# Kernel optimization log

Hardware: AMD Instinct MI355X
Metric: run time of the kernel (lower is better)

Reference implementation:

```python
import jax, jax.numpy as jnp
import numpy as np

N = 20        # number_of_nodes
K = 2         # Chebyshev order
E_DIM = 4     # embedding_dimensions
OUT = 2       # out_channels
F_IN = 8      # node_features
B = 131072    # batch


def setup_inputs() -> dict:
    key = jax.random.key(0)
    ks = jax.random.split(key, 8)
    x = jax.random.normal(ks[0], (B, N, F_IN), jnp.float32)
    e = jax.random.normal(ks[1], (N, E_DIM), jnp.float32)
    # AVWGCN parameter pools: weights_pool (E_DIM, K, in, out), bias_pool (E_DIM, out)
    gate_w = jax.random.normal(ks[2], (E_DIM, K, F_IN + OUT, 2 * OUT), jnp.float32) * 0.1
    gate_b = jax.random.normal(ks[3], (E_DIM, 2 * OUT), jnp.float32) * 0.1
    upd_w = jax.random.normal(ks[4], (E_DIM, K, F_IN + OUT, OUT), jnp.float32) * 0.1
    upd_b = jax.random.normal(ks[5], (E_DIM, OUT), jnp.float32) * 0.1
    lin_w = jax.random.normal(ks[6], (1, OUT), jnp.float32) * 0.5
    lin_b = jax.random.normal(ks[7], (1,), jnp.float32) * 0.1
    return {"x": x, "e": e, "gate_w": gate_w, "gate_b": gate_b,
            "upd_w": upd_w, "upd_b": upd_b, "lin_w": lin_w, "lin_b": lin_b}


def _avwgcn(x, e, supports, w_pool, b_pool):
    # Node-adaptive weights: (N, K, in, out) and bias (N, out)
    W = jnp.einsum('nd,dkio->nkio', e, w_pool)
    b = e @ b_pool
    # K-hop graph conv gather: (B, N, K, in)
    x_g = jnp.einsum('knm,bmc->bnkc', supports, x)
    return jnp.einsum('bnki,nkio->bno', x_g, W) + b


def reference(x, e, gate_w, gate_b, upd_w, upd_b, lin_w, lin_b):
    dt = x.dtype
    # Adaptive adjacency: softmax(relu(E E^T)) rows; Chebyshev set for K=2 is [I, A]
    A = jax.nn.softmax(jax.nn.relu(e @ e.T), axis=1)
    supports = jnp.stack([jnp.eye(N, dtype=dt), A.astype(dt)])  # (K, N, N)

    H = jnp.zeros((x.shape[0], N, OUT), dt)  # self.h is None -> zeros
    XH = jnp.concatenate([x, H], axis=-1)
    ZR = jax.nn.sigmoid(_avwgcn(XH, e, supports, gate_w, gate_b))
    Z, R = ZR[..., :OUT], ZR[..., OUT:]
    C = jnp.concatenate([x, Z * H], axis=-1)
    HC = jnp.tanh(_avwgcn(C, e, supports, upd_w, upd_b))
    H = R * H + (1.0 - R) * HC

    y = jax.nn.relu(H)
    y = y @ lin_w.T + lin_b
    return y
```

## Files before the change

### kernel.cpp

```cpp
#include <hip/hip_runtime.h>
#include <math.h>

#define NN 20
#define ED 4
#define XROW 160
#define NC 80
#define NKT 5
#define NNT 5
#define FRAG_BYTES (NKT * NNT * 64 * 16)
#define THREADS 512
#define ROWS_PER_WAVE 16
#define ROWS_PER_BLOCK 128
#define TPB 2

typedef __attribute__((ext_vector_type(8))) _Float16 half8;
typedef __attribute__((ext_vector_type(4))) float f32x4;
typedef __attribute__((ext_vector_type(4))) unsigned uint4v;

static __device__ __forceinline__ half8 cvt8(float4 a, float4 b) {
    uint4v u = (uint4v){
        __builtin_bit_cast(unsigned, __builtin_amdgcn_cvt_pkrtz(a.x, a.y)),
        __builtin_bit_cast(unsigned, __builtin_amdgcn_cvt_pkrtz(a.z, a.w)),
        __builtin_bit_cast(unsigned, __builtin_amdgcn_cvt_pkrtz(b.x, b.y)),
        __builtin_bit_cast(unsigned, __builtin_amdgcn_cvt_pkrtz(b.z, b.w))};
    return __builtin_bit_cast(half8, u);
}

static __device__ __forceinline__ float dpp_xor1(float v) {
    return __builtin_bit_cast(float,
        __builtin_amdgcn_mov_dpp(__builtin_bit_cast(int, v), 0xB1, 0xF, 0xF, true));
}
static __device__ __forceinline__ float dpp_xor2(float v) {
    return __builtin_bit_cast(float,
        __builtin_amdgcn_mov_dpp(__builtin_bit_cast(int, v), 0x4E, 0xF, 0xF, true));
}

struct Burst {
    float4 a0, b0, a1, b1, a2, b2, a3, b3, a4, b4;
};

static __device__ __forceinline__ Burst load_burst(const float* __restrict__ p) {
    Burst r;
    r.a0 = *(const float4*)(p);        r.b0 = *(const float4*)(p + 16);
    r.a1 = *(const float4*)(p + 32);   r.b1 = *(const float4*)(p + 48);
    r.a2 = *(const float4*)(p + 64);   r.b2 = *(const float4*)(p + 80);
    r.a3 = *(const float4*)(p + 96);   r.b3 = *(const float4*)(p + 112);
    r.a4 = *(const float4*)(p + 128);  r.b4 = *(const float4*)(p + 144);
    return r;
}

__global__ __launch_bounds__(THREADS, 4) void rgcn_fused(
        const float* __restrict__ x,
        const float* __restrict__ e,
        const float* __restrict__ gate_w,
        const float* __restrict__ gate_b,
        const float* __restrict__ upd_w,
        const float* __restrict__ upd_b,
        const float* __restrict__ lin_w,
        const float* __restrict__ lin_b,
        float* __restrict__ y) {
    __shared__ __align__(16) char fragmem[FRAG_BYTES];
    __shared__ float sbias[NC];
    __shared__ float el[80];
    __shared__ float sA[400];
    __shared__ float wself[640];
    __shared__ float wagg[640];

    const int t = threadIdx.x;
    const int l = t & 63;
    const int w = t >> 6;

    const size_t rowA = ((size_t)blockIdx.x * TPB + 0) * ROWS_PER_BLOCK + (size_t)w * ROWS_PER_WAVE;
    const size_t rowB = ((size_t)blockIdx.x * TPB + 1) * ROWS_PER_BLOCK + (size_t)w * ROWS_PER_WAVE;
    const float* xpA = x + (rowA + (l & 15)) * XROW + ((l >> 4) << 2);
    const float* xpB = x + (rowB + (l & 15)) * XROW + ((l >> 4) << 2);

    Burst bA = load_burst(xpA);

    if (t < NN * ED) el[t] = e[t];
    __syncthreads();

    if (t < 400) {
        int nn = t / 20, mm = t - (t / 20) * 20;
        float d = 0.f;
        #pragma unroll
        for (int j = 0; j < ED; ++j) d += el[nn * ED + j] * el[mm * ED + j];
        sA[t] = fmaxf(d, 0.f);
    }
    #pragma unroll
    for (int idx = t; idx < 1280; idx += THREADS) {
        int sel = idx >= 640;
        int rem = sel ? idx - 640 : idx;
        int c = rem >> 3, i = rem & 7;
        int n = c >> 2, ro = c & 3;
        float v = 0.f;
        if (ro < 2) {
            int o = 2 + ro;
            #pragma unroll
            for (int d = 0; d < ED; ++d) v += el[n * ED + d] * gate_w[d * 80 + sel * 40 + i * 4 + o];
        } else {
            int o = ro - 2;
            #pragma unroll
            for (int d = 0; d < ED; ++d) v += el[n * ED + d] * upd_w[d * 40 + sel * 20 + i * 2 + o];
        }
        (sel ? wagg : wself)[rem] = v;
    }
    if (t < NC) {
        int n = t >> 2, ro = t & 3;
        float b = 0.f;
        #pragma unroll
        for (int d = 0; d < ED; ++d)
            b += el[n * ED + d] * (ro < 2 ? gate_b[d * 4 + 2 + ro] : upd_b[d * 2 + ro - 2]);
        sbias[t] = b;
    }
    __syncthreads();

    if (t < NN) {
        float mx = -1e30f;
        for (int m = 0; m < NN; ++m) mx = fmaxf(mx, sA[t * 20 + m]);
        float ex[NN]; float sum = 0.f;
        for (int m = 0; m < NN; ++m) { ex[m] = __expf(sA[t * 20 + m] - mx); sum += ex[m]; }
        float inv = 1.f / sum;
        for (int m = 0; m < NN; ++m) sA[t * 20 + m] = ex[m] * inv;
    }
    __syncthreads();

    {
        half8* frag = (half8*)fragmem;
        const int gg = l >> 4;
        for (int tile = w; tile < NKT * NNT; tile += 8) {
            int kt = tile / 5, nt = tile - kt * 5;
            int cc = nt * 16 + (l & 15);
            int nn = cc >> 2;
            half8 hv;
            #pragma unroll
            for (int j = 0; j < 8; ++j) {
                int kk = (j < 4) ? (gg * 4 + j) : (16 + gg * 4 + (j - 4));
                int k = kt * 32 + kk;
                int m = k >> 3, i = k & 7;
                float val = sA[nn * 20 + m] * wagg[cc * 8 + i]
                          + (nn == m ? wself[cc * 8 + i] : 0.f);
                hv[j] = (_Float16)val;
            }
            frag[tile * 64 + l] = hv;
        }
    }
    __syncthreads();

    const half8* frag = (const half8*)fragmem;
    const float lw0 = lin_w[0], lw1 = lin_w[1], lb = lin_b[0];
    const int ro = l & 3;
    const bool isR = ro < 2;
    const float myw = (ro & 1) ? lw1 : lw0;

    Burst bB = load_burst(xpB);

    #define STEP(XA, XB, KT, ACC)                                                   \
    {                                                                               \
        half8 a = cvt8(XA, XB);                                                     \
        _Pragma("unroll")                                                           \
        for (int nt = 0; nt < NNT; ++nt) {                                          \
            half8 bh = frag[((KT) * NNT + nt) * 64 + l];                            \
            ACC[nt] = __builtin_amdgcn_mfma_f32_16x16x32_f16(a, bh, ACC[nt], 0, 0, 0); \
        }                                                                           \
    }

    #define EPILOGUE(ACC, ROW0)                                                     \
    {                                                                               \
        const size_t rowb = (ROW0) + ((l >> 4) << 2) + ro;                          \
        _Pragma("unroll")                                                           \
        for (int nt = 0; nt < NNT; ++nt) {                                          \
            const int n = nt * 4 + ((l & 15) >> 2);                                 \
            float ysel = 0.f;                                                       \
            _Pragma("unroll")                                                       \
            for (int q = 0; q < 4; ++q) {                                           \
                float pre = ACC[nt][q];                                             \
                float term;                                                         \
                if (isR) term = __builtin_amdgcn_rcpf(1.f + __expf(pre));           \
                else     term = 1.f - 2.f * __builtin_amdgcn_rcpf(__expf(2.f * pre) + 1.f); \
                float other = dpp_xor2(term);                                       \
                float h = term * other;                                             \
                float s = fmaxf(h, 0.f) * myw;                                      \
                float yq = s + dpp_xor1(s) + lb;                                    \
                if (q == ro) ysel = yq;                                             \
            }                                                                       \
            y[rowb * NN + n] = ysel;                                                \
        }                                                                           \
    }

    {
        f32x4 accA[NNT];
        #pragma unroll
        for (int nt = 0; nt < NNT; ++nt) {
            float b = sbias[nt * 16 + (l & 15)];
            accA[nt] = (f32x4){b, b, b, b};
        }
        STEP(bA.a0, bA.b0, 0, accA)
        STEP(bA.a1, bA.b1, 1, accA)
        STEP(bA.a2, bA.b2, 2, accA)
        STEP(bA.a3, bA.b3, 3, accA)
        STEP(bA.a4, bA.b4, 4, accA)
        EPILOGUE(accA, rowA)
    }

    {
        f32x4 accB[NNT];
        #pragma unroll
        for (int nt = 0; nt < NNT; ++nt) {
            float b = sbias[nt * 16 + (l & 15)];
            accB[nt] = (f32x4){b, b, b, b};
        }
        STEP(bB.a0, bB.b0, 0, accB)
        STEP(bB.a1, bB.b1, 1, accB)
        STEP(bB.a2, bB.b2, 2, accB)
        STEP(bB.a3, bB.b3, 3, accB)
        STEP(bB.a4, bB.b4, 4, accB)
        EPILOGUE(accB, rowB)
    }
    #undef STEP
    #undef EPILOGUE
}

extern "C" void kernel_launch(void* const* d_in, const int* in_sizes, int n_in,
                              void* d_out, int out_size, void* d_ws, size_t ws_size,
                              hipStream_t stream) {
    const float* x      = (const float*)d_in[0];
    const float* e      = (const float*)d_in[1];
    const float* gate_w = (const float*)d_in[2];
    const float* gate_b = (const float*)d_in[3];
    const float* upd_w  = (const float*)d_in[4];
    const float* upd_b  = (const float*)d_in[5];
    const float* lin_w  = (const float*)d_in[6];
    const float* lin_b  = (const float*)d_in[7];
    float* y = (float*)d_out;

    const int Bn = in_sizes[0] / XROW;
    const int nblocks = Bn / (ROWS_PER_BLOCK * TPB);

    rgcn_fused<<<nblocks, THREADS, 0, stream>>>(x, e, gate_w, gate_b,
                                                upd_w, upd_b, lin_w, lin_b, y);
}
```

Measured before the change: 25.43 us.

## Overlap x loads and weight prefetch with setup using no-drain barriers

```diff
diff --git a/kernel.cpp b/kernel.cpp
--- a/kernel.cpp
+++ b/kernel.cpp
@@ -35,17 +35,24 @@
         __builtin_amdgcn_mov_dpp(__builtin_bit_cast(int, v), 0x4E, 0xF, 0xF, true));
 }
 
+#define BARRIER_NODRAIN()                                   \
+    do {                                                    \
+        asm volatile("s_waitcnt lgkmcnt(0)" ::: "memory");  \
+        __builtin_amdgcn_s_barrier();                       \
+        __builtin_amdgcn_sched_barrier(0);                  \
+    } while (0)
+
 struct Burst {
     float4 a0, b0, a1, b1, a2, b2, a3, b3, a4, b4;
 };
 
 static __device__ __forceinline__ Burst load_burst(const float* __restrict__ p) {
     Burst r;
-    r.a0 = *(const float4*)(p);        r.b0 = *(const float4*)(p + 16);
-    r.a1 = *(const float4*)(p + 32);   r.b1 = *(const float4*)(p + 48);
-    r.a2 = *(const float4*)(p + 64);   r.b2 = *(const float4*)(p + 80);
-    r.a3 = *(const float4*)(p + 96);   r.b3 = *(const float4*)(p + 112);
-    r.a4 = *(const float4*)(p + 128);  r.b4 = *(const float4*)(p + 144);
+    r.a0 = *(const float4*)(p);       r.b0 = *(const float4*)(p + 4);
+    r.a1 = *(const float4*)(p + 32);  r.b1 = *(const float4*)(p + 36);
+    r.a2 = *(const float4*)(p + 64);  r.b2 = *(const float4*)(p + 68);
+    r.a3 = *(const float4*)(p + 96);  r.b3 = *(const float4*)(p + 100);
+    r.a4 = *(const float4*)(p + 128); r.b4 = *(const float4*)(p + 132);
     return r;
 }
 
@@ -72,13 +79,47 @@
 
     const size_t rowA = ((size_t)blockIdx.x * TPB + 0) * ROWS_PER_BLOCK + (size_t)w * ROWS_PER_WAVE;
     const size_t rowB = ((size_t)blockIdx.x * TPB + 1) * ROWS_PER_BLOCK + (size_t)w * ROWS_PER_WAVE;
-    const float* xpA = x + (rowA + (l & 15)) * XROW + ((l >> 4) << 2);
-    const float* xpB = x + (rowB + (l & 15)) * XROW + ((l >> 4) << 2);
+    const float* xpA = x + (rowA + (l & 15)) * XROW + ((l >> 4) << 3);
+    const float* xpB = x + (rowB + (l & 15)) * XROW + ((l >> 4) << 3);
+
+    const float lw0 = lin_w[0], lw1 = lin_w[1], lb = lin_b[0];
+
+    float ev = 0.f;
+    if (t < NN * ED) ev = e[t];
+
+    float q0a[ED], q1a[ED];
+    {
+        int c = t >> 3, i = t & 7, ro = c & 3;
+        const float* b0; const float* b1; int st;
+        if (ro < 2) { b0 = gate_w + i * 4 + 2 + ro; b1 = b0 + 40; st = 80; }
+        else        { b0 = upd_w  + i * 2 + ro - 2; b1 = b0 + 20; st = 40; }
+        #pragma unroll
+        for (int d = 0; d < ED; ++d) { q0a[d] = b0[d * st]; q1a[d] = b1[d * st]; }
+    }
+    float q0b[ED], q1b[ED];
+    if (t < 128) {
+        int rem = t + 512;
+        int c = rem >> 3, i = rem & 7, ro = c & 3;
+        const float* b0; const float* b1; int st;
+        if (ro < 2) { b0 = gate_w + i * 4 + 2 + ro; b1 = b0 + 40; st = 80; }
+        else        { b0 = upd_w  + i * 2 + ro - 2; b1 = b0 + 20; st = 40; }
+        #pragma unroll
+        for (int d = 0; d < ED; ++d) { q0b[d] = b0[d * st]; q1b[d] = b1[d * st]; }
+    }
+    float pb[ED];
+    if (t < NC) {
+        int rb = t & 3;
+        #pragma unroll
+        for (int d = 0; d < ED; ++d)
+            pb[d] = (rb < 2) ? gate_b[d * 4 + 2 + rb] : upd_b[d * 2 + rb - 2];
+    }
 
     Burst bA = load_burst(xpA);
-
-    if (t < NN * ED) el[t] = e[t];
-    __syncthreads();
+    Burst bB = load_burst(xpB);
+    __builtin_amdgcn_sched_barrier(0);
+
+    if (t < NN * ED) el[t] = ev;
+    BARRIER_NODRAIN();
 
     if (t < 400) {
         int nn = t / 20, mm = t - (t / 20) * 20;
@@ -87,33 +128,37 @@
         for (int j = 0; j < ED; ++j) d += el[nn * ED + j] * el[mm * ED + j];
         sA[t] = fmaxf(d, 0.f);
     }
-    #pragma unroll
-    for (int idx = t; idx < 1280; idx += THREADS) {
-        int sel = idx >= 640;
-        int rem = sel ? idx - 640 : idx;
-        int c = rem >> 3, i = rem & 7;
-        int n = c >> 2, ro = c & 3;
-        float v = 0.f;
-        if (ro < 2) {
-            int o = 2 + ro;
-            #pragma unroll
-            for (int d = 0; d < ED; ++d) v += el[n * ED + d] * gate_w[d * 80 + sel * 40 + i * 4 + o];
-        } else {
-            int o = ro - 2;
-            #pragma unroll
-            for (int d = 0; d < ED; ++d) v += el[n * ED + d] * upd_w[d * 40 + sel * 20 + i * 2 + o];
-        }
-        (sel ? wagg : wself)[rem] = v;
+    {
+        int n1 = t >> 5;
+        float vs = 0.f, va = 0.f;
+        #pragma unroll
+        for (int d = 0; d < ED; ++d) {
+            float evd = el[n1 * ED + d];
+            vs += evd * q0a[d];
+            va += evd * q1a[d];
+        }
+        wself[t] = vs;
+        wagg[t]  = va;
+    }
+    if (t < 128) {
+        int rem = t + 512, n2 = rem >> 5;
+        float vs = 0.f, va = 0.f;
+        #pragma unroll
+        for (int d = 0; d < ED; ++d) {
+            float evd = el[n2 * ED + d];
+            vs += evd * q0b[d];
+            va += evd * q1b[d];
+        }
+        wself[rem] = vs;
+        wagg[rem]  = va;
     }
     if (t < NC) {
-        int n = t >> 2, ro = t & 3;
         float b = 0.f;
         #pragma unroll
-        for (int d = 0; d < ED; ++d)
-            b += el[n * ED + d] * (ro < 2 ? gate_b[d * 4 + 2 + ro] : upd_b[d * 2 + ro - 2]);
+        for (int d = 0; d < ED; ++d) b += el[(t >> 2) * ED + d] * pb[d];
         sbias[t] = b;
     }
-    __syncthreads();
+    BARRIER_NODRAIN();
 
     if (t < NN) {
         float mx = -1e30f;
@@ -123,37 +168,38 @@
         float inv = 1.f / sum;
         for (int m = 0; m < NN; ++m) sA[t * 20 + m] = ex[m] * inv;
     }
-    __syncthreads();
+    BARRIER_NODRAIN();
 
     {
         half8* frag = (half8*)fragmem;
-        const int gg = l >> 4;
         for (int tile = w; tile < NKT * NNT; tile += 8) {
             int kt = tile / 5, nt = tile - kt * 5;
             int cc = nt * 16 + (l & 15);
             int nn = cc >> 2;
+            int mm = kt * 4 + (l >> 4);
+            float anm = sA[nn * 20 + mm];
+            float4 wg0 = *(const float4*)&wagg[cc * 8];
+            float4 wg1 = *(const float4*)&wagg[cc * 8 + 4];
+            float v0 = anm * wg0.x, v1 = anm * wg0.y, v2 = anm * wg0.z, v3 = anm * wg0.w;
+            float v4 = anm * wg1.x, v5 = anm * wg1.y, v6 = anm * wg1.z, v7 = anm * wg1.w;
+            if (nn == mm) {
+                float4 ws0 = *(const float4*)&wself[cc * 8];
+                float4 ws1 = *(const float4*)&wself[cc * 8 + 4];
+                v0 += ws0.x; v1 += ws0.y; v2 += ws0.z; v3 += ws0.w;
+                v4 += ws1.x; v5 += ws1.y; v6 += ws1.z; v7 += ws1.w;
+            }
             half8 hv;
-            #pragma unroll
-            for (int j = 0; j < 8; ++j) {
-                int kk = (j < 4) ? (gg * 4 + j) : (16 + gg * 4 + (j - 4));
-                int k = kt * 32 + kk;
-                int m = k >> 3, i = k & 7;
-                float val = sA[nn * 20 + m] * wagg[cc * 8 + i]
-                          + (nn == m ? wself[cc * 8 + i] : 0.f);
-                hv[j] = (_Float16)val;
-            }
+            hv[0] = (_Float16)v0; hv[1] = (_Float16)v1; hv[2] = (_Float16)v2; hv[3] = (_Float16)v3;
+            hv[4] = (_Float16)v4; hv[5] = (_Float16)v5; hv[6] = (_Float16)v6; hv[7] = (_Float16)v7;
             frag[tile * 64 + l] = hv;
         }
     }
-    __syncthreads();
+    BARRIER_NODRAIN();
 
     const half8* frag = (const half8*)fragmem;
-    const float lw0 = lin_w[0], lw1 = lin_w[1], lb = lin_b[0];
     const int ro = l & 3;
     const bool isR = ro < 2;
     const float myw = (ro & 1) ? lw1 : lw0;
-
-    Burst bB = load_burst(xpB);
 
     #define STEP(XA, XB, KT, ACC)                                                   \
     {                                                                               \
```

After: 25.20 us. About the same (-0.9%).
